# Performance work log

Measured on AMD Instinct MI355X. Metric: run time of the kernel, lower is better.

## Reference

```python
import jax, jax.numpy as jnp
import numpy as np

B, H, W, C = 8, 64, 64, 256
NUM_GROUPS = 32
EPS = 1e-6  # flax GroupNorm default


def setup_inputs() -> dict:
    key = jax.random.key(0)
    ks = jax.random.split(key, 9)
    x = jax.random.normal(ks[0], (B, H, W, C), dtype=jnp.float32)
    init = lambda k, shape: jax.random.normal(k, shape, dtype=jnp.float32) * 0.02
    return {
        "x": x,
        "gn_scale": jnp.ones((C,), jnp.float32),
        "gn_bias": jnp.zeros((C,), jnp.float32),
        "wq": init(ks[1], (C, C)), "bq": jnp.zeros((C,), jnp.float32),
        "wk": init(ks[2], (C, C)), "bk": jnp.zeros((C,), jnp.float32),
        "wv": init(ks[3], (C, C)), "bv": jnp.zeros((C,), jnp.float32),
        "wo": init(ks[4], (C, C)), "bo": jnp.zeros((C,), jnp.float32),
    }


def group_norm(x, scale, bias, num_groups, eps):
    b, h, w, c = x.shape
    xg = x.reshape(b, h, w, num_groups, c // num_groups)
    mean = jnp.mean(xg, axis=(1, 2, 4), keepdims=True)
    var = jnp.mean(jnp.square(xg - mean), axis=(1, 2, 4), keepdims=True)
    xn = (xg - mean) * jax.lax.rsqrt(var + eps)
    return xn.reshape(b, h, w, c) * scale + bias


def reference(x, gn_scale, gn_bias, wq, bq, wk, bk, wv, bv, wo, bo):
    b, h, w, c = x.shape
    hn = group_norm(x, gn_scale, gn_bias, NUM_GROUPS, EPS)
    hf = hn.reshape(b, h * w, c)  # (B, S, C)
    q = hf @ wq + bq
    k = hf @ wk + bk
    v = hf @ wv + bv
    scaling = jnp.sqrt(jnp.float32(c)).astype(x.dtype)
    attn = jax.nn.softmax(jnp.einsum('bsc,btc->bst', q, k) / scaling, axis=-1)
    out = jnp.einsum('bst,btc->bsc', attn, v)
    out = out @ wo + bo
    return out.reshape(b, h, w, c) + x
```

## Files before the change

### kernel.cpp

```cpp
#include <hip/hip_runtime.h>

#define NB   8
#define SS   4096
#define CC   256
#define NG   32
#define CPG  8
#define EPSV 1e-6f
#define MTOT (NB * SS)

typedef short bf16x8 __attribute__((ext_vector_type(8)));
typedef float f32x4  __attribute__((ext_vector_type(4)));
typedef float f32x16 __attribute__((ext_vector_type(16)));
typedef int   i32x4  __attribute__((ext_vector_type(4)));
typedef int   i32x8  __attribute__((ext_vector_type(8)));
typedef unsigned char u8;

typedef __attribute__((address_space(1))) const unsigned int as1_u32;
typedef __attribute__((address_space(3))) unsigned int as3_u32;

__device__ __forceinline__ unsigned short f2bf(float f) {
  unsigned int u = __builtin_bit_cast(unsigned int, f);
  u = (u + 0x7FFFu + ((u >> 16) & 1u)) >> 16;
  return (unsigned short)u;
}
__device__ __forceinline__ u8 f2fp8(float f) {
  return (u8)(__builtin_amdgcn_cvt_pk_fp8_f32(f, f, 0, 0) & 0xFF);
}
__device__ __forceinline__ void dma16(const u8* src, u8* lds) {
  __builtin_amdgcn_global_load_lds((as1_u32*)src, (as3_u32*)lds, 16, 0, 0);
}

__global__ __launch_bounds__(256) void gn_stats_kernel(const float* __restrict__ x,
                                                       float* __restrict__ stats) {
  int bg = blockIdx.x;
  int b = bg >> 5, g = bg & 31;
  const float* base = x + (size_t)b * SS * CC + g * CPG;
  float s = 0.f, ss = 0.f;
  for (int pos = threadIdx.x; pos < SS; pos += 256) {
    const float4* p = (const float4*)(base + (size_t)pos * CC);
    float4 a = p[0];
    float4 c = p[1];
    s  += (a.x + a.y) + (a.z + a.w) + (c.x + c.y) + (c.z + c.w);
    ss += (a.x*a.x + a.y*a.y) + (a.z*a.z + a.w*a.w)
        + (c.x*c.x + c.y*c.y) + (c.z*c.z + c.w*c.w);
  }
#pragma unroll
  for (int off = 32; off >= 1; off >>= 1) {
    s  += __shfl_xor(s, off);
    ss += __shfl_xor(ss, off);
  }
  __shared__ float rs[4], rss[4];
  int wv = threadIdx.x >> 6;
  if ((threadIdx.x & 63) == 0) { rs[wv] = s; rss[wv] = ss; }
  __syncthreads();
  if (threadIdx.x == 0) {
    float ts  = (rs[0] + rs[1]) + (rs[2] + rs[3]);
    float tss = (rss[0] + rss[1]) + (rss[2] + rss[3]);
    const float inv = 1.f / (float)(SS * CPG);
    float mean = ts * inv;
    float var  = tss * inv - mean * mean;
    stats[bg * 2]     = mean;
    stats[bg * 2 + 1] = rsqrtf(var + EPSV);
  }
}

__global__ __launch_bounds__(256) void gn_norm_kernel(const float* __restrict__ x,
                                                      const float* __restrict__ stats,
                                                      const float* __restrict__ gamma,
                                                      const float* __restrict__ beta,
                                                      unsigned short* __restrict__ hn) {
  int i4 = blockIdx.x * 256 + threadIdx.x;
  int c4 = (i4 & 63) * 4;
  size_t row = (size_t)(i4 >> 6);
  int b = (int)(row >> 12);
  int sidx = (b * NG + (c4 >> 3)) * 2;
  float mean = stats[sidx], rstd = stats[sidx + 1];
  float4 v  = *(const float4*)(x + row * CC + c4);
  float4 ga = *(const float4*)(gamma + c4);
  float4 be = *(const float4*)(beta + c4);
  ushort4 o;
  o.x = f2bf((v.x - mean) * rstd * ga.x + be.x);
  o.y = f2bf((v.y - mean) * rstd * ga.y + be.y);
  o.z = f2bf((v.z - mean) * rstd * ga.z + be.z);
  o.w = f2bf((v.w - mean) * rstd * ga.w + be.w);
  *(ushort4*)(hn + row * CC + c4) = o;
}

__global__ __launch_bounds__(256) void prep_wt_kernel(
    const float* __restrict__ w0, const float* __restrict__ w1,
    const float* __restrict__ w2, const float* __restrict__ w3,
    unsigned short* __restrict__ wt) {
  __shared__ float t[64][68];
  int which = blockIdx.y;
  const float* W = (which == 0) ? w0 : (which == 1) ? w1 : (which == 2) ? w2 : w3;
  int tx = (blockIdx.x & 3) * 64;
  int ty = (blockIdx.x >> 2) * 64;
  int tid = threadIdx.x;
  int row = tid >> 4;
  int col = (tid & 15) * 4;
#pragma unroll
  for (int i = 0; i < 4; i++) {
    float4 v = *(const float4*)(W + (size_t)(ty + row + i * 16) * CC + tx + col);
    *(float4*)(&t[row + i * 16][col]) = v;
  }
  __syncthreads();
#pragma unroll
  for (int i = 0; i < 4; i++) {
    int n = row + i * 16;
    ushort4 o;
    o.x = f2bf(t[col + 0][n]);
    o.y = f2bf(t[col + 1][n]);
    o.z = f2bf(t[col + 2][n]);
    o.w = f2bf(t[col + 3][n]);
    *(ushort4*)(wt + (size_t)which * CC * CC + (size_t)(tx + n) * CC + ty + col) = o;
  }
}

#define XTM 256
#define XTN 64
#define XTK 32
#define XLD 40

__global__ __launch_bounds__(256) void qkv_gemm_kernel(
    const unsigned short* __restrict__ A,
    const unsigned short* __restrict__ WT,
    const float* __restrict__ bq, const float* __restrict__ bk, const float* __restrict__ bv,
    u8* __restrict__ qo, u8* __restrict__ ko, u8* __restrict__ vt) {
  __shared__ unsigned short As[XTM * XLD];
  __shared__ unsigned short Bs[XTN * XLD];

  const int which = blockIdx.z;
  const unsigned short* Bw = WT + (size_t)which * CC * CC;
  const float* bias = (which == 0) ? bq : (which == 1) ? bk : bv;

  const int m0 = blockIdx.x * XTM;
  const int n0 = blockIdx.y * XTN;
  const int tid = threadIdx.x;
  const int wave = tid >> 6, lane = tid & 63;
  const int l32 = lane & 31, h = lane >> 5;

  const int srow = tid >> 2, schunk = (tid & 3) * 8;
  const unsigned short* Ab = A  + (size_t)(m0 + srow) * CC + schunk;
  const unsigned short* Bb = Bw + (size_t)(n0 + srow) * CC + schunk;

  bf16x8 astg[4], bstg;
#pragma unroll
  for (int i = 0; i < 4; i++) astg[i] = *(const bf16x8*)(Ab + (size_t)i * 64 * CC);
  bstg = *(const bf16x8*)(Bb);

  f32x16 acc[2][2] = {};
  const int abase = (wave * 64 + l32) * XLD + h * 8;
  const int bbase = l32 * XLD + h * 8;

  for (int k0 = 0; k0 < CC; k0 += XTK) {
    __syncthreads();
#pragma unroll
    for (int i = 0; i < 4; i++)
      *(bf16x8*)(&As[(srow + i * 64) * XLD + schunk]) = astg[i];
    *(bf16x8*)(&Bs[srow * XLD + schunk]) = bstg;
    __syncthreads();

    if (k0 + XTK < CC) {
      int kn = k0 + XTK;
#pragma unroll
      for (int i = 0; i < 4; i++) astg[i] = *(const bf16x8*)(Ab + kn + (size_t)i * 64 * CC);
      bstg = *(const bf16x8*)(Bb + kn);
    }

#pragma unroll
    for (int ks = 0; ks < 2; ks++) {
      bf16x8 af0 = *(const bf16x8*)(&As[abase + ks * 16]);
      bf16x8 af1 = *(const bf16x8*)(&As[abase + 32 * XLD + ks * 16]);
      bf16x8 bf0 = *(const bf16x8*)(&Bs[bbase + ks * 16]);
      bf16x8 bf1 = *(const bf16x8*)(&Bs[bbase + 32 * XLD + ks * 16]);
      acc[0][0] = __builtin_amdgcn_mfma_f32_32x32x16_bf16(af0, bf0, acc[0][0], 0, 0, 0);
      acc[0][1] = __builtin_amdgcn_mfma_f32_32x32x16_bf16(af0, bf1, acc[0][1], 0, 0, 0);
      acc[1][0] = __builtin_amdgcn_mfma_f32_32x32x16_bf16(af1, bf0, acc[1][0], 0, 0, 0);
      acc[1][1] = __builtin_amdgcn_mfma_f32_32x32x16_bf16(af1, bf1, acc[1][1], 0, 0, 0);
    }
  }

  if (which < 2) {
    u8* out = (which == 0) ? qo : ko;
#pragma unroll
    for (int nt = 0; nt < 2; nt++) {
      int n = n0 + nt * 32 + l32;
      float bv_ = bias[n];
#pragma unroll
      for (int mt = 0; mt < 2; mt++)
#pragma unroll
        for (int r = 0; r < 16; r++) {
          int m = m0 + wave * 64 + mt * 32 + (r & 3) + 8 * (r >> 2) + 4 * h;
          out[(size_t)m * CC + n] = f2fp8(acc[mt][nt][r] + bv_);
        }
    }
  } else {
    int bb = m0 >> 12;
#pragma unroll
    for (int nt = 0; nt < 2; nt++) {
      int n = n0 + nt * 32 + l32;
      float bv_ = bias[n];
#pragma unroll
      for (int mt = 0; mt < 2; mt++)
#pragma unroll
        for (int g = 0; g < 4; g++) {
          int mg = m0 + wave * 64 + mt * 32 + g * 8 + 4 * h;
          int w = __builtin_amdgcn_cvt_pk_fp8_f32(acc[mt][nt][g*4+0] + bv_, acc[mt][nt][g*4+1] + bv_, 0, 0);
          w = __builtin_amdgcn_cvt_pk_fp8_f32(acc[mt][nt][g*4+2] + bv_, acc[mt][nt][g*4+3] + bv_, w, 1);
          *(unsigned int*)(vt + (size_t)bb * CC * SS + (size_t)n * SS + (mg & 4095)) = (unsigned int)w;
        }
    }
  }
}

__global__ __launch_bounds__(256) void out_gemm_kernel(
    const unsigned short* __restrict__ A,
    const unsigned short* __restrict__ WT,
    const float* __restrict__ bias,
    const float* __restrict__ residual,
    float* __restrict__ Of) {
  __shared__ unsigned short As[XTM * XLD];
  __shared__ unsigned short Bs[XTN * XLD];

  const unsigned short* Bw = WT + (size_t)3 * CC * CC;
  const int m0 = blockIdx.x * XTM;
  const int n0 = blockIdx.y * XTN;
  const int tid = threadIdx.x;
  const int wave = tid >> 6, lane = tid & 63;
  const int l32 = lane & 31, h = lane >> 5;

  const int srow = tid >> 2, schunk = (tid & 3) * 8;
  const unsigned short* Ab = A  + (size_t)(m0 + srow) * CC + schunk;
  const unsigned short* Bb = Bw + (size_t)(n0 + srow) * CC + schunk;

  bf16x8 astg[4], bstg;
#pragma unroll
  for (int i = 0; i < 4; i++) astg[i] = *(const bf16x8*)(Ab + (size_t)i * 64 * CC);
  bstg = *(const bf16x8*)(Bb);

  f32x16 acc[2][2] = {};
  const int abase = (wave * 64 + l32) * XLD + h * 8;
  const int bbase = l32 * XLD + h * 8;

  for (int k0 = 0; k0 < CC; k0 += XTK) {
    __syncthreads();
#pragma unroll
    for (int i = 0; i < 4; i++)
      *(bf16x8*)(&As[(srow + i * 64) * XLD + schunk]) = astg[i];
    *(bf16x8*)(&Bs[srow * XLD + schunk]) = bstg;
    __syncthreads();

    if (k0 + XTK < CC) {
      int kn = k0 + XTK;
#pragma unroll
      for (int i = 0; i < 4; i++) astg[i] = *(const bf16x8*)(Ab + kn + (size_t)i * 64 * CC);
      bstg = *(const bf16x8*)(Bb + kn);
    }

#pragma unroll
    for (int ks = 0; ks < 2; ks++) {
      bf16x8 af0 = *(const bf16x8*)(&As[abase + ks * 16]);
      bf16x8 af1 = *(const bf16x8*)(&As[abase + 32 * XLD + ks * 16]);
      bf16x8 bf0 = *(const bf16x8*)(&Bs[bbase + ks * 16]);
      bf16x8 bf1 = *(const bf16x8*)(&Bs[bbase + 32 * XLD + ks * 16]);
      acc[0][0] = __builtin_amdgcn_mfma_f32_32x32x16_bf16(af0, bf0, acc[0][0], 0, 0, 0);
      acc[0][1] = __builtin_amdgcn_mfma_f32_32x32x16_bf16(af0, bf1, acc[0][1], 0, 0, 0);
      acc[1][0] = __builtin_amdgcn_mfma_f32_32x32x16_bf16(af1, bf0, acc[1][0], 0, 0, 0);
      acc[1][1] = __builtin_amdgcn_mfma_f32_32x32x16_bf16(af1, bf1, acc[1][1], 0, 0, 0);
    }
  }

#pragma unroll
  for (int nt = 0; nt < 2; nt++) {
    int n = n0 + nt * 32 + l32;
    float bv_ = bias[n];
#pragma unroll
    for (int mt = 0; mt < 2; mt++)
#pragma unroll
      for (int r = 0; r < 16; r++) {
        int m = m0 + wave * 64 + mt * 32 + (r & 3) + 8 * (r >> 2) + 4 * h;
        Of[(size_t)m * CC + n] = acc[mt][nt][r] + bv_ + residual[(size_t)m * CC + n];
      }
  }
}

#define BR 64

__global__ __launch_bounds__(256, 2) void flash_attn_kernel(
    const u8* __restrict__ Qg,
    const u8* __restrict__ Kg,
    const u8* __restrict__ Vtg,
    unsigned short* __restrict__ Og) {
  __shared__ __align__(1024) u8 smem[65536 + 512];
  u8* KA  = smem;
  u8* KBb = smem + 16384;
  u8* VB  = smem + 32768;

  const int bid = blockIdx.x;
  const int b = bid & 7, q0 = (bid >> 3) * BR;
  const int tid = threadIdx.x;
  const int wave = tid >> 6, lane = tid & 63;
  const int l32 = lane & 31, h = lane >> 5;
  const int wm = wave >> 1, wn = wave & 1;

  const u8* Qb  = Qg  + (size_t)b * SS * CC;
  const u8* Kb  = Kg  + (size_t)b * SS * CC;
  const u8* Vtb = Vtg + (size_t)b * CC * SS;

  const int kkey = tid >> 4, kc16 = tid & 15;
  const u8* ksrc0 = Kb + (size_t)kkey * CC + ((kc16 ^ (kkey & 15)) << 4);
  const int vch = tid >> 3;
  const int vs  = (tid & 7) ^ (vch & 7);
  const u8* vsrc0 = Vtb + (size_t)vch * SS + (vs << 4);

  i32x8 qf[4];
  {
    const u8* qrow = Qb + (size_t)(q0 + wm * 32 + l32) * CC + h * 32;
#pragma unroll
    for (int t = 0; t < 4; t++) qf[t] = *(const i32x8*)(qrow + t * 64);
  }

  f32x16 oacc[8] = {};
  float ll = 0.f;

#pragma unroll
  for (int i = 0; i < 4; i++)
    dma16(ksrc0 + (size_t)i * 16 * CC, KA + i * 4096 + tid * 16);

  const int kswz = l32 & 15;
  const int vswz = l32 & 7;

  for (int jp = 0; jp < 32; ++jp) {
    int w0[4], w1[4];

    __syncthreads();
    {
      size_t krow = (size_t)jp * 128 + 64;
#pragma unroll
      for (int i = 0; i < 4; i++)
        dma16(ksrc0 + (krow + (size_t)i * 16) * CC, KBb + i * 4096 + tid * 16);
      size_t vbase = (size_t)jp * 128;
#pragma unroll
      for (int i = 0; i < 8; i++)
        dma16(vsrc0 + (size_t)i * 32 * SS + vbase, VB + i * 4096 + tid * 16);
    }
    {
      f32x16 sacc = {};
      const u8* kb = KA + (wn * 32 + l32) * 256;
#pragma unroll
      for (int t = 0; t < 4; t++) {
        i32x4 r0 = *(const i32x4*)(kb + (((t * 4 + 2 * h)     ^ kswz) << 4));
        i32x4 r1 = *(const i32x4*)(kb + (((t * 4 + 2 * h + 1) ^ kswz) << 4));
        i32x8 kf = __builtin_shufflevector(r0, r1, 0, 1, 2, 3, 4, 5, 6, 7);
        sacc = __builtin_amdgcn_mfma_scale_f32_32x32x64_f8f6f4(
            kf, qf[t], sacc, 0, 0, 0, 0x7F7F7F7F, 0, 0x7F7F7F7F);
      }
#pragma unroll
      for (int g = 0; g < 4; g++) {
        float p0 = exp2f(fminf(sacc[g * 4 + 0] * 0.09016844f, 7.213475f));
        float p1 = exp2f(fminf(sacc[g * 4 + 1] * 0.09016844f, 7.213475f));
        float p2 = exp2f(fminf(sacc[g * 4 + 2] * 0.09016844f, 7.213475f));
        float p3 = exp2f(fminf(sacc[g * 4 + 3] * 0.09016844f, 7.213475f));
        ll += (p0 + p1) + (p2 + p3);
        int wv_ = __builtin_amdgcn_cvt_pk_fp8_f32(p0, p1, 0, 0);
        w0[g] = __builtin_amdgcn_cvt_pk_fp8_f32(p2, p3, wv_, 1);
      }
    }

    __syncthreads();
    if (jp + 1 < 32) {
      size_t krow = (size_t)(jp + 1) * 128;
#pragma unroll
      for (int i = 0; i < 4; i++)
        dma16(ksrc0 + (krow + (size_t)i * 16) * CC, KA + i * 4096 + tid * 16);
    }
    {
      f32x16 sacc = {};
      const u8* kb = KBb + (wn * 32 + l32) * 256;
#pragma unroll
      for (int t = 0; t < 4; t++) {
        i32x4 r0 = *(const i32x4*)(kb + (((t * 4 + 2 * h)     ^ kswz) << 4));
        i32x4 r1 = *(const i32x4*)(kb + (((t * 4 + 2 * h + 1) ^ kswz) << 4));
        i32x8 kf = __builtin_shufflevector(r0, r1, 0, 1, 2, 3, 4, 5, 6, 7);
        sacc = __builtin_amdgcn_mfma_scale_f32_32x32x64_f8f6f4(
            kf, qf[t], sacc, 0, 0, 0, 0x7F7F7F7F, 0, 0x7F7F7F7F);
      }
#pragma unroll
      for (int g = 0; g < 4; g++) {
        float p0 = exp2f(fminf(sacc[g * 4 + 0] * 0.09016844f, 7.213475f));
        float p1 = exp2f(fminf(sacc[g * 4 + 1] * 0.09016844f, 7.213475f));
        float p2 = exp2f(fminf(sacc[g * 4 + 2] * 0.09016844f, 7.213475f));
        float p3 = exp2f(fminf(sacc[g * 4 + 3] * 0.09016844f, 7.213475f));
        ll += (p0 + p1) + (p2 + p3);
        int wv_ = __builtin_amdgcn_cvt_pk_fp8_f32(p0, p1, 0, 0);
        w1[g] = __builtin_amdgcn_cvt_pk_fp8_f32(p2, p3, wv_, 1);
      }
    }

    int pa_[8];
#pragma unroll
    for (int g = 0; g < 4; g++) {
      int o1 = __shfl_xor(w1[g], 32);
      int o0 = __shfl_xor(w0[g], 32);
      pa_[2 * g]     = (h == 0) ? w0[g] : o1;
      pa_[2 * g + 1] = (h == 0) ? o0 : w1[g];
    }
    i32x8 pa = {pa_[0], pa_[1], pa_[2], pa_[3], pa_[4], pa_[5], pa_[6], pa_[7]};

#pragma unroll
    for (int nt = 0; nt < 8; nt++) {
      const u8* vb = VB + (nt * 32 + l32) * 128;
      i32x4 r0 = *(const i32x4*)(vb + (((4 * h + 2 * wn)     ^ vswz) << 4));
      i32x4 r1 = *(const i32x4*)(vb + (((4 * h + 2 * wn + 1) ^ vswz) << 4));
      i32x8 vf = __builtin_shufflevector(r0, r1, 0, 1, 2, 3, 4, 5, 6, 7);
      oacc[nt] = __builtin_amdgcn_mfma_scale_f32_32x32x64_f8f6f4(
          pa, vf, oacc[nt], 0, 0, 0, 0x7F7F7F7F, 0, 0x7F7F7F7F);
    }
  }

  __syncthreads();
  ll += __shfl_xor(ll, 32);
  float* Lred = (float*)(smem + 65536);
  if (h == 0) Lred[wn * 64 + wm * 32 + l32] = ll;

  float* scratch = (float*)smem;
  {
    float* z = scratch + (size_t)(wm * 2 + (1 - wn)) * 4096;
#pragma unroll
    for (int ntg = 0; ntg < 8; ntg++) {
      if ((ntg >> 2) != wn) {
        int nt = ntg & 3;
#pragma unroll
        for (int r = 0; r < 16; r++) {
          int row = (r & 3) + 8 * (r >> 2) + 4 * h;
          z[row * 128 + nt * 32 + l32] = oacc[ntg][r];
        }
      }
    }
  }
  __syncthreads();
  {
    const float* z = scratch + (size_t)(wm * 2 + wn) * 4096;
#pragma unroll
    for (int ntg = 0; ntg < 8; ntg++) {
      if ((ntg >> 2) == wn) {
        int nt = ntg & 3;
#pragma unroll
        for (int r = 0; r < 16; r++) {
          int row = (r & 3) + 8 * (r >> 2) + 4 * h;
          float inv = 1.f / (Lred[wm * 32 + row] + Lred[64 + wm * 32 + row]);
          float v = oacc[ntg][r] + z[row * 128 + nt * 32 + l32];
          Og[((size_t)b * SS + q0 + wm * 32 + row) * CC + wn * 128 + nt * 32 + l32]
              = f2bf(v * inv);
        }
      }
    }
  }
}

extern "C" void kernel_launch(void* const* d_in, const int* in_sizes, int n_in,
                              void* d_out, int out_size, void* d_ws, size_t ws_size,
                              hipStream_t stream) {
  const float* x   = (const float*)d_in[0];
  const float* gsc = (const float*)d_in[1];
  const float* gbi = (const float*)d_in[2];
  const float* wq  = (const float*)d_in[3];
  const float* bq  = (const float*)d_in[4];
  const float* wk  = (const float*)d_in[5];
  const float* bk  = (const float*)d_in[6];
  const float* wv  = (const float*)d_in[7];
  const float* bv  = (const float*)d_in[8];
  const float* wo  = (const float*)d_in[9];
  const float* bo  = (const float*)d_in[10];
  float* out = (float*)d_out;

  char* ws = (char*)d_ws;
  const size_t MAT = (size_t)MTOT * CC;
  float* stats        = (float*)ws;
  unsigned short* wt  = (unsigned short*)(ws + 4096);
  unsigned short* hn  = wt + (size_t)4 * CC * CC;
  unsigned short* ao  = hn + MAT;
  u8* q  = (u8*)(ao + MAT);
  u8* k  = q + MAT;
  u8* vt = k + MAT;

  gn_stats_kernel<<<NB * NG, 256, 0, stream>>>(x, stats);
  prep_wt_kernel<<<dim3(16, 4), 256, 0, stream>>>(wq, wk, wv, wo, wt);
  gn_norm_kernel<<<(int)(MAT / 4 / 256), 256, 0, stream>>>(x, stats, gsc, gbi, hn);

  qkv_gemm_kernel<<<dim3(MTOT / XTM, CC / XTN, 3), 256, 0, stream>>>(
      hn, wt, bq, bk, bv, q, k, vt);

  flash_attn_kernel<<<NB * (SS / BR), 256, 0, stream>>>(q, k, vt, ao);

  out_gemm_kernel<<<dim3(MTOT / XTM, CC / XTN), 256, 0, stream>>>(ao, wt, bo, x, out);
}
```

Before: 275.3 us.

## Tune flash attention scheduling, use native exp2, widen GN stats blocks

Wraps the attention MFMA loops in s_setprio to favour matrix-issuing waves. Replaces exp2f with the hardware exp2 builtin. Moves the first cross-half shuffle earlier to overlap it with the second score block. Also raises the group-norm stats kernel from 256 to 1024 threads per block so each of the 256 blocks has more memory parallelism. Together these are several unrelated micro-optimisations. The native exp2 may differ slightly in accuracy and denormal handling.

```diff
diff --git a/kernel.cpp b/kernel.cpp
--- a/kernel.cpp
+++ b/kernel.cpp
@@ -29,14 +29,21 @@
 __device__ __forceinline__ void dma16(const u8* src, u8* lds) {
   __builtin_amdgcn_global_load_lds((as1_u32*)src, (as3_u32*)lds, 16, 0, 0);
 }
-
-__global__ __launch_bounds__(256) void gn_stats_kernel(const float* __restrict__ x,
-                                                       float* __restrict__ stats) {
+__device__ __forceinline__ float fast_exp2(float x) {
+#if __has_builtin(__builtin_amdgcn_exp2f)
+  return __builtin_amdgcn_exp2f(x);
+#else
+  return exp2f(x);
+#endif
+}
+
+__global__ __launch_bounds__(1024) void gn_stats_kernel(const float* __restrict__ x,
+                                                        float* __restrict__ stats) {
   int bg = blockIdx.x;
   int b = bg >> 5, g = bg & 31;
   const float* base = x + (size_t)b * SS * CC + g * CPG;
   float s = 0.f, ss = 0.f;
-  for (int pos = threadIdx.x; pos < SS; pos += 256) {
+  for (int pos = threadIdx.x; pos < SS; pos += 1024) {
     const float4* p = (const float4*)(base + (size_t)pos * CC);
     float4 a = p[0];
     float4 c = p[1];
@@ -49,13 +56,14 @@
     s  += __shfl_xor(s, off);
     ss += __shfl_xor(ss, off);
   }
-  __shared__ float rs[4], rss[4];
+  __shared__ float rs[16], rss[16];
   int wv = threadIdx.x >> 6;
   if ((threadIdx.x & 63) == 0) { rs[wv] = s; rss[wv] = ss; }
   __syncthreads();
   if (threadIdx.x == 0) {
-    float ts  = (rs[0] + rs[1]) + (rs[2] + rs[3]);
-    float tss = (rss[0] + rss[1]) + (rss[2] + rss[3]);
+    float ts = 0.f, tss = 0.f;
+#pragma unroll
+    for (int i = 0; i < 16; i++) { ts += rs[i]; tss += rss[i]; }
     const float inv = 1.f / (float)(SS * CPG);
     float mean = ts * inv;
     float var  = tss * inv - mean * mean;
@@ -331,7 +339,7 @@
   const int vswz = l32 & 7;
 
   for (int jp = 0; jp < 32; ++jp) {
-    int w0[4], w1[4];
+    int w0[4], w1[4], o0[4];
 
     __syncthreads();
     {
@@ -347,6 +355,7 @@
     {
       f32x16 sacc = {};
       const u8* kb = KA + (wn * 32 + l32) * 256;
+      __builtin_amdgcn_s_setprio(1);
 #pragma unroll
       for (int t = 0; t < 4; t++) {
         i32x4 r0 = *(const i32x4*)(kb + (((t * 4 + 2 * h)     ^ kswz) << 4));
@@ -355,16 +364,19 @@
         sacc = __builtin_amdgcn_mfma_scale_f32_32x32x64_f8f6f4(
             kf, qf[t], sacc, 0, 0, 0, 0x7F7F7F7F, 0, 0x7F7F7F7F);
       }
+      __builtin_amdgcn_s_setprio(0);
 #pragma unroll
       for (int g = 0; g < 4; g++) {
-        float p0 = exp2f(fminf(sacc[g * 4 + 0] * 0.09016844f, 7.213475f));
-        float p1 = exp2f(fminf(sacc[g * 4 + 1] * 0.09016844f, 7.213475f));
-        float p2 = exp2f(fminf(sacc[g * 4 + 2] * 0.09016844f, 7.213475f));
-        float p3 = exp2f(fminf(sacc[g * 4 + 3] * 0.09016844f, 7.213475f));
+        float p0 = fast_exp2(fminf(sacc[g * 4 + 0] * 0.09016844f, 7.213475f));
+        float p1 = fast_exp2(fminf(sacc[g * 4 + 1] * 0.09016844f, 7.213475f));
+        float p2 = fast_exp2(fminf(sacc[g * 4 + 2] * 0.09016844f, 7.213475f));
+        float p3 = fast_exp2(fminf(sacc[g * 4 + 3] * 0.09016844f, 7.213475f));
         ll += (p0 + p1) + (p2 + p3);
         int wv_ = __builtin_amdgcn_cvt_pk_fp8_f32(p0, p1, 0, 0);
         w0[g] = __builtin_amdgcn_cvt_pk_fp8_f32(p2, p3, wv_, 1);
       }
+#pragma unroll
+      for (int g = 0; g < 4; g++) o0[g] = __shfl_xor(w0[g], 32);
     }
 
     __syncthreads();
@@ -377,6 +389,7 @@
     {
       f32x16 sacc = {};
       const u8* kb = KBb + (wn * 32 + l32) * 256;
+      __builtin_amdgcn_s_setprio(1);
 #pragma unroll
       for (int t = 0; t < 4; t++) {
         i32x4 r0 = *(const i32x4*)(kb + (((t * 4 + 2 * h)     ^ kswz) << 4));
@@ -385,12 +398,13 @@
         sacc = __builtin_amdgcn_mfma_scale_f32_32x32x64_f8f6f4(
             kf, qf[t], sacc, 0, 0, 0, 0x7F7F7F7F, 0, 0x7F7F7F7F);
       }
+      __builtin_amdgcn_s_setprio(0);
 #pragma unroll
       for (int g = 0; g < 4; g++) {
-        float p0 = exp2f(fminf(sacc[g * 4 + 0] * 0.09016844f, 7.213475f));
-        float p1 = exp2f(fminf(sacc[g * 4 + 1] * 0.09016844f, 7.213475f));
-        float p2 = exp2f(fminf(sacc[g * 4 + 2] * 0.09016844f, 7.213475f));
-        float p3 = exp2f(fminf(sacc[g * 4 + 3] * 0.09016844f, 7.213475f));
+        float p0 = fast_exp2(fminf(sacc[g * 4 + 0] * 0.09016844f, 7.213475f));
+        float p1 = fast_exp2(fminf(sacc[g * 4 + 1] * 0.09016844f, 7.213475f));
+        float p2 = fast_exp2(fminf(sacc[g * 4 + 2] * 0.09016844f, 7.213475f));
+        float p3 = fast_exp2(fminf(sacc[g * 4 + 3] * 0.09016844f, 7.213475f));
         ll += (p0 + p1) + (p2 + p3);
         int wv_ = __builtin_amdgcn_cvt_pk_fp8_f32(p0, p1, 0, 0);
         w1[g] = __builtin_amdgcn_cvt_pk_fp8_f32(p2, p3, wv_, 1);
@@ -401,12 +415,12 @@
 #pragma unroll
     for (int g = 0; g < 4; g++) {
       int o1 = __shfl_xor(w1[g], 32);
-      int o0 = __shfl_xor(w0[g], 32);
       pa_[2 * g]     = (h == 0) ? w0[g] : o1;
-      pa_[2 * g + 1] = (h == 0) ? o0 : w1[g];
+      pa_[2 * g + 1] = (h == 0) ? o0[g] : w1[g];
     }
     i32x8 pa = {pa_[0], pa_[1], pa_[2], pa_[3], pa_[4], pa_[5], pa_[6], pa_[7]};
 
+    __builtin_amdgcn_s_setprio(1);
 #pragma unroll
     for (int nt = 0; nt < 8; nt++) {
       const u8* vb = VB + (nt * 32 + l32) * 128;
@@ -416,6 +430,7 @@
       oacc[nt] = __builtin_amdgcn_mfma_scale_f32_32x32x64_f8f6f4(
           pa, vf, oacc[nt], 0, 0, 0, 0x7F7F7F7F, 0, 0x7F7F7F7F);
     }
+    __builtin_amdgcn_s_setprio(0);
   }
 
   __syncthreads();
@@ -484,7 +499,7 @@
   u8* k  = q + MAT;
   u8* vt = k + MAT;
 
-  gn_stats_kernel<<<NB * NG, 256, 0, stream>>>(x, stats);
+  gn_stats_kernel<<<NB * NG, 1024, 0, stream>>>(x, stats);
   prep_wt_kernel<<<dim3(16, 4), 256, 0, stream>>>(wq, wk, wv, wo, wt);
   gn_norm_kernel<<<(int)(MAT / 4 / 256), 256, 0, stream>>>(x, stats, gsc, gbi, hn);
 
```

After: 262.0 us. 4.8% less time.
